# Performance work log

Hardware: AMD Instinct MI355X
Metric: run time of the kernel (lower is better)

Reference implementation:

```python
import jax, jax.numpy as jnp
import numpy as np

N = 10000   # nodes
E = 80000   # edges
B = 2       # batch
T = 12      # time steps
F_IN = 64
F_OUT = 64


def setup_inputs() -> dict:
    key = jax.random.key(0)
    ks = jax.random.split(key, 8)
    x = jax.random.normal(ks[0], (B, N, T, F_IN), dtype=jnp.float32)
    src = jax.random.randint(ks[1], (E,), 0, N)
    dst = jax.random.randint(ks[2], (E,), 0, N)
    s = 1.0 / np.sqrt(F_IN)
    W_pool = jax.random.uniform(ks[3], (F_IN, F_IN), jnp.float32, -s, s)
    b_pool = jax.random.uniform(ks[4], (F_IN,), jnp.float32, -s, s)
    W_neigh = jax.random.uniform(ks[5], (F_OUT, F_IN), jnp.float32, -s, s)
    W_self = jax.random.uniform(ks[6], (F_OUT, F_IN), jnp.float32, -s, s)
    bias = jnp.zeros((F_OUT,), jnp.float32)
    return dict(x=x, src=src, dst=dst, W_pool=W_pool, b_pool=b_pool,
                W_neigh=W_neigh, W_self=W_self, bias=bias)


def reference(x, src, dst, W_pool, b_pool, W_neigh, W_self, bias):
    # x: (B, N, T, F) -> (N, B, T, F); node dim first as SAGEConv expects
    h = jnp.transpose(x, (1, 0, 2, 3))
    # pool aggregator: per-node MLP + relu (done on nodes, then gathered per edge
    # -- identical math to gather-then-MLP since the MLP is per-node/elementwise)
    msg = jax.nn.relu(jnp.einsum('nbtf,gf->nbtg', h, W_pool) + b_pool)  # (N,B,T,F)
    m = msg[src]                                                        # (E,B,T,F) gather
    neigh = jax.ops.segment_max(m, dst, num_segments=N)                 # max-pool per dst node
    # zero-in-degree nodes get -inf from segment_max -> replace with 0 (DGL behavior)
    neigh = jnp.where(jnp.isfinite(neigh), neigh, jnp.zeros((), neigh.dtype))
    rst = (jnp.einsum('nbtf,of->nbto', h, W_self)
           + jnp.einsum('nbtf,of->nbto', neigh, W_neigh)
           + bias)                                                      # (N,B,T,F_OUT)
    return jnp.transpose(rst, (1, 0, 2, 3))                              # (B,N,T,F_OUT)
```

## Files before the change

### kernel.cpp

```cpp
#include <hip/hip_runtime.h>

#define NN 10000
#define NE 80000
#define NB 2
#define NT 12
#define NF 64
#define ROWS (NB*NN*NT)

typedef __attribute__((ext_vector_type(8))) short bf16x8;
typedef __attribute__((ext_vector_type(4))) float f32x4;

__device__ __forceinline__ unsigned short f2b(float f) {
    unsigned int u = __builtin_bit_cast(unsigned int, f);
    u += 0x7fffu + ((u >> 16) & 1u);
    return (unsigned short)(u >> 16);
}
__device__ __forceinline__ float b2f_lo(unsigned int u){ return __builtin_bit_cast(float, u << 16); }
__device__ __forceinline__ float b2f_hi(unsigned int u){ return __builtin_bit_cast(float, u & 0xffff0000u); }

__global__ __launch_bounds__(256) void k_prep(const float* __restrict__ Wp,
        const float* __restrict__ Wn, const float* __restrict__ Ws,
        unsigned short* __restrict__ Wp_b, unsigned short* __restrict__ Wcat) {
    int t = threadIdx.x;
    for (int i = t; i < 4096; i += 256) {
        Wp_b[i] = f2b(Wp[i]);
        int o = i >> 6, g = i & 63;
        Wcat[o*128 + g] = f2b(Ws[i]);
        Wcat[o*128 + 64 + ((g & 15)*4 + (g >> 4))] = f2b(Wn[i]);
    }
}

__global__ __launch_bounds__(256) void k_msg(const float* __restrict__ x,
        const unsigned short* __restrict__ Wp_b, const float* __restrict__ bp,
        unsigned short* __restrict__ msg, unsigned short* __restrict__ xb) {
    __shared__ __align__(16) unsigned short A[128*72];
    __shared__ __align__(16) unsigned short W[64*72];
    int tid = threadIdx.x;
    {
        int row = tid >> 2, c = (tid & 3) * 16;
        bf16x8 w0 = *(const bf16x8*)(Wp_b + row*64 + c);
        bf16x8 w1 = *(const bf16x8*)(Wp_b + row*64 + c + 8);
        *(bf16x8*)(W + row*72 + c)     = w0;
        *(bf16x8*)(W + row*72 + c + 8) = w1;
    }
    int m0 = blockIdx.x * 128;
    #pragma unroll
    for (int k = 0; k < 8; ++k) {
        int c = tid + 256*k;
        int row = c >> 4, f0 = (c & 15) * 4;
        float4 v = *(const float4*)(x + (size_t)(m0 + row)*64 + f0);
        uint2 p;
        p.x = f2b(v.x) | ((unsigned int)f2b(v.y) << 16);
        p.y = f2b(v.z) | ((unsigned int)f2b(v.w) << 16);
        *(uint2*)(A + row*72 + f0) = p;
        *(uint2*)(xb + (size_t)(m0 + row)*64 + f0) = p;
    }
    __syncthreads();

    int lane = tid & 63, w = tid >> 6;
    int cl = lane & 15, gq = lane >> 4;
    f32x4 acc[2][4] = {};
    #pragma unroll
    for (int kk = 0; kk < 2; ++kk) {
        int ko = kk*32 + gq*8;
        bf16x8 a0 = *(const bf16x8*)(A + (w*32 + cl)*72 + ko);
        bf16x8 a1 = *(const bf16x8*)(A + (w*32 + 16 + cl)*72 + ko);
        #pragma unroll
        for (int nf = 0; nf < 4; ++nf) {
            bf16x8 b = *(const bf16x8*)(W + (nf*16 + cl)*72 + ko);
            acc[0][nf] = __builtin_amdgcn_mfma_f32_16x16x32_bf16(a0, b, acc[0][nf], 0,0,0);
            acc[1][nf] = __builtin_amdgcn_mfma_f32_16x16x32_bf16(a1, b, acc[1][nf], 0,0,0);
        }
    }
    float bpv[4];
    #pragma unroll
    for (int nf = 0; nf < 4; ++nf) bpv[nf] = bp[nf*16 + cl];
    #pragma unroll
    for (int m = 0; m < 2; ++m)
    #pragma unroll
    for (int r = 0; r < 4; ++r) {
        int row = m0 + w*32 + m*16 + gq*4 + r;
        int b  = row / (NN*NT);
        int rem = row - b*(NN*NT);
        int node = rem / NT, t = rem - node*NT;
        float v0 = fmaxf(acc[m][0][r] + bpv[0], 0.f);
        float v1 = fmaxf(acc[m][1][r] + bpv[1], 0.f);
        float v2 = fmaxf(acc[m][2][r] + bpv[2], 0.f);
        float v3 = fmaxf(acc[m][3][r] + bpv[3], 0.f);
        uint2 p;
        p.x = f2b(v0) | ((unsigned int)f2b(v1) << 16);
        p.y = f2b(v2) | ((unsigned int)f2b(v3) << 16);
        *(uint2*)(msg + ((size_t)(node*24 + b*12 + t)*64) + cl*4) = p;
    }
}

__global__ void k_count(const int* __restrict__ dst, int* __restrict__ cnt) {
    int e = blockIdx.x * blockDim.x + threadIdx.x;
    if (e < NE) atomicAdd(&cnt[dst[e]], 1);
}

__global__ __launch_bounds__(1024) void k_scan(const int* __restrict__ cnt,
        int* __restrict__ rowptr, int* __restrict__ wofs) {
    __shared__ int s[1024];
    int tid = threadIdx.x;
    const int C = 10;
    int base = tid * C;
    int loc[C];
    int sum = 0;
    for (int i = 0; i < C; ++i) {
        int idx = base + i;
        int v = (idx < NN) ? cnt[idx] : 0;
        loc[i] = sum;
        sum += v;
    }
    s[tid] = sum;
    __syncthreads();
    for (int off = 1; off < 1024; off <<= 1) {
        int v = (tid >= off) ? s[tid - off] : 0;
        __syncthreads();
        s[tid] += v;
        __syncthreads();
    }
    int prev = (tid == 0) ? 0 : s[tid - 1];
    for (int i = 0; i < C; ++i) {
        int idx = base + i;
        if (idx < NN) {
            int v = prev + loc[i];
            rowptr[idx] = v;
            wofs[idx]   = v;
        }
    }
    if (tid == 1023) rowptr[NN] = s[1023];
}

__global__ void k_scatter(const int* __restrict__ src, const int* __restrict__ dst,
        int* __restrict__ wofs, int* __restrict__ csr) {
    int e = blockIdx.x * blockDim.x + threadIdx.x;
    if (e < NE) {
        int pos = atomicAdd(&wofs[dst[e]], 1);
        csr[pos] = src[e];
    }
}

__global__ __launch_bounds__(256, 8) void k_out(const unsigned short* __restrict__ xb,
        const unsigned short* __restrict__ msg, const unsigned short* __restrict__ Wcat,
        const float* __restrict__ bias,
        const int* __restrict__ rowptr, const int* __restrict__ csr,
        float* __restrict__ out) {
    __shared__ __align__(16) unsigned short A[32*136];
    int tid = threadIdx.x;
    int n = blockIdx.x;

    {
        int c = tid, row = c >> 4, f0 = (c & 15) * 4;
        int b = row / 12, tt = row - b*12;
        *(uint2*)(A + row*136 + f0) =
            *(const uint2*)(xb + ((size_t)(b*NN + n)*12 + tt)*64 + f0);
        if (tid < 128) {
            int c2 = tid + 256, row2 = c2 >> 4, f02 = (c2 & 15)*4;
            int b2 = row2 / 12, tt2 = row2 - b2*12;
            *(uint2*)(A + row2*136 + f02) =
                *(const uint2*)(xb + ((size_t)(b2*NN + n)*12 + tt2)*64 + f02);
        } else {
            unsigned int* z = (unsigned int*)(A + 24*136);
            int i = tid - 128;
            #pragma unroll
            for (int k = 0; k < 5; ++k) { int j = i + 128*k; if (j < 544) z[j] = 0u; }
        }
    }
    const unsigned int* msg_dw = (const unsigned int*)msg;
    int rp0 = rowptr[n], rp1 = rowptr[n + 1];
    int i0 = tid, i1 = tid + 256, i2 = tid + 512;
    float mlo[3] = {0.f,0.f,0.f}, mhi[3] = {0.f,0.f,0.f};
    int e = rp0;
    for (; e + 4 <= rp1; e += 4) {
        int s0 = csr[e]*768, s1 = csr[e+1]*768, s2 = csr[e+2]*768, s3 = csr[e+3]*768;
        unsigned int u00 = msg_dw[s0+i0], u01 = msg_dw[s0+i1], u02 = msg_dw[s0+i2];
        unsigned int u10 = msg_dw[s1+i0], u11 = msg_dw[s1+i1], u12 = msg_dw[s1+i2];
        unsigned int u20 = msg_dw[s2+i0], u21 = msg_dw[s2+i1], u22 = msg_dw[s2+i2];
        unsigned int u30 = msg_dw[s3+i0], u31 = msg_dw[s3+i1], u32 = msg_dw[s3+i2];
        mlo[0] = fmaxf(fmaxf(fmaxf(mlo[0], b2f_lo(u00)), fmaxf(b2f_lo(u10), b2f_lo(u20))), b2f_lo(u30));
        mhi[0] = fmaxf(fmaxf(fmaxf(mhi[0], b2f_hi(u00)), fmaxf(b2f_hi(u10), b2f_hi(u20))), b2f_hi(u30));
        mlo[1] = fmaxf(fmaxf(fmaxf(mlo[1], b2f_lo(u01)), fmaxf(b2f_lo(u11), b2f_lo(u21))), b2f_lo(u31));
        mhi[1] = fmaxf(fmaxf(fmaxf(mhi[1], b2f_hi(u01)), fmaxf(b2f_hi(u11), b2f_hi(u21))), b2f_hi(u31));
        mlo[2] = fmaxf(fmaxf(fmaxf(mlo[2], b2f_lo(u02)), fmaxf(b2f_lo(u12), b2f_lo(u22))), b2f_lo(u32));
        mhi[2] = fmaxf(fmaxf(fmaxf(mhi[2], b2f_hi(u02)), fmaxf(b2f_hi(u12), b2f_hi(u22))), b2f_hi(u32));
    }
    for (; e < rp1; ++e) {
        int s0 = csr[e]*768;
        unsigned int u0 = msg_dw[s0+i0], u1 = msg_dw[s0+i1], u2 = msg_dw[s0+i2];
        mlo[0] = fmaxf(mlo[0], b2f_lo(u0));  mhi[0] = fmaxf(mhi[0], b2f_hi(u0));
        mlo[1] = fmaxf(mlo[1], b2f_lo(u1));  mhi[1] = fmaxf(mhi[1], b2f_hi(u1));
        mlo[2] = fmaxf(mlo[2], b2f_lo(u2));  mhi[2] = fmaxf(mhi[2], b2f_hi(u2));
    }
    {
        unsigned int lo0 = __builtin_bit_cast(unsigned int, mlo[0]) >> 16;
        unsigned int hi0 = __builtin_bit_cast(unsigned int, mhi[0]) & 0xffff0000u;
        *(unsigned int*)(A + (i0>>5)*136 + 64 + (i0&31)*2) = hi0 | lo0;
        unsigned int lo1 = __builtin_bit_cast(unsigned int, mlo[1]) >> 16;
        unsigned int hi1 = __builtin_bit_cast(unsigned int, mhi[1]) & 0xffff0000u;
        *(unsigned int*)(A + (i1>>5)*136 + 64 + (i1&31)*2) = hi1 | lo1;
        unsigned int lo2 = __builtin_bit_cast(unsigned int, mlo[2]) >> 16;
        unsigned int hi2 = __builtin_bit_cast(unsigned int, mhi[2]) & 0xffff0000u;
        *(unsigned int*)(A + (i2>>5)*136 + 64 + (i2&31)*2) = hi2 | lo2;
    }
    __syncthreads();

    int lane = tid & 63, w = tid >> 6;
    int cl = lane & 15, gq = lane >> 4;
    f32x4 acc0 = {}, acc1 = {};
    #pragma unroll
    for (int kk = 0; kk < 4; ++kk) {
        int ko = kk*32 + gq*8;
        bf16x8 b  = *(const bf16x8*)(Wcat + (w*16 + cl)*128 + ko);
        bf16x8 a0 = *(const bf16x8*)(A + cl*136 + ko);
        bf16x8 a1 = *(const bf16x8*)(A + (16 + cl)*136 + ko);
        acc0 = __builtin_amdgcn_mfma_f32_16x16x32_bf16(a0, b, acc0, 0,0,0);
        acc1 = __builtin_amdgcn_mfma_f32_16x16x32_bf16(a1, b, acc1, 0,0,0);
    }
    float bv = bias[w*16 + cl];
    #pragma unroll
    for (int r = 0; r < 4; ++r) {
        int row = gq*4 + r;
        int b0 = row / 12, tt = row - b0*12;
        out[((size_t)(b0*NN + n)*12 + tt)*64 + w*16 + cl] = acc0[r] + bv;
    }
    if (gq < 2) {
        #pragma unroll
        for (int r = 0; r < 4; ++r) {
            int row = 16 + gq*4 + r;
            int b0 = row / 12, tt = row - b0*12;
            out[((size_t)(b0*NN + n)*12 + tt)*64 + w*16 + cl] = acc1[r] + bv;
        }
    }
}

extern "C" void kernel_launch(void* const* d_in, const int* in_sizes, int n_in,
                              void* d_out, int out_size, void* d_ws, size_t ws_size,
                              hipStream_t stream) {
    const float* x    = (const float*)d_in[0];
    const int*   src  = (const int*)  d_in[1];
    const int*   dst  = (const int*)  d_in[2];
    const float* Wp   = (const float*)d_in[3];
    const float* bp   = (const float*)d_in[4];
    const float* Wn   = (const float*)d_in[5];
    const float* Wsf  = (const float*)d_in[6];
    const float* bias = (const float*)d_in[7];
    float* out = (float*)d_out;

    char* ws = (char*)d_ws;
    int*            cnt    = (int*)           (ws);
    int*            rowptr = (int*)           (ws + 40064);
    int*            wofs   = (int*)           (ws + 80128);
    int*            csr    = (int*)           (ws + 120192);
    unsigned short* Wp_b   = (unsigned short*)(ws + 440320);
    unsigned short* Wcat   = (unsigned short*)(ws + 448512);
    unsigned short* msg    = (unsigned short*)(ws + 464896);
    unsigned short* xb     = (unsigned short*)(ws + 31184896);

    hipMemsetAsync(cnt, 0, NN * sizeof(int), stream);
    k_prep   <<<1, 256, 0, stream>>>(Wp, Wn, Wsf, Wp_b, Wcat);
    k_msg    <<<ROWS/128, 256, 0, stream>>>(x, Wp_b, bp, msg, xb);
    k_count  <<<(NE + 255) / 256, 256, 0, stream>>>(dst, cnt);
    k_scan   <<<1, 1024, 0, stream>>>(cnt, rowptr, wofs);
    k_scatter<<<(NE + 255) / 256, 256, 0, stream>>>(src, dst, wofs, csr);
    k_out    <<<NN, 256, 0, stream>>>(xb, msg, Wcat, bias, rowptr, csr, out);
}
```

Measured before the change: 107.4 us.

## Process one node per wavefront in output kernel with packed bf16 integer max

```diff
diff --git a/kernel.cpp b/kernel.cpp
--- a/kernel.cpp
+++ b/kernel.cpp
@@ -8,6 +8,7 @@
 #define ROWS (NB*NN*NT)
 
 typedef __attribute__((ext_vector_type(8))) short bf16x8;
+typedef __attribute__((ext_vector_type(8))) unsigned short u16x8;
 typedef __attribute__((ext_vector_type(4))) float f32x4;
 
 __device__ __forceinline__ unsigned short f2b(float f) {
@@ -15,8 +16,6 @@
     u += 0x7fffu + ((u >> 16) & 1u);
     return (unsigned short)(u >> 16);
 }
-__device__ __forceinline__ float b2f_lo(unsigned int u){ return __builtin_bit_cast(float, u << 16); }
-__device__ __forceinline__ float b2f_hi(unsigned int u){ return __builtin_bit_cast(float, u & 0xffff0000u); }
 
 __global__ __launch_bounds__(256) void k_prep(const float* __restrict__ Wp,
         const float* __restrict__ Wn, const float* __restrict__ Ws,
@@ -48,12 +47,16 @@
     for (int k = 0; k < 8; ++k) {
         int c = tid + 256*k;
         int row = c >> 4, f0 = (c & 15) * 4;
-        float4 v = *(const float4*)(x + (size_t)(m0 + row)*64 + f0);
+        int grow = m0 + row;
+        float4 v = *(const float4*)(x + (size_t)grow*64 + f0);
         uint2 p;
         p.x = f2b(v.x) | ((unsigned int)f2b(v.y) << 16);
         p.y = f2b(v.z) | ((unsigned int)f2b(v.w) << 16);
         *(uint2*)(A + row*72 + f0) = p;
-        *(uint2*)(xb + (size_t)(m0 + row)*64 + f0) = p;
+        int b = grow / (NN*NT);
+        int rem = grow - b*(NN*NT);
+        int node = rem / NT, t = rem - node*NT;
+        *(uint2*)(xb + ((size_t)node*24 + b*12 + t)*64 + f0) = p;
     }
     __syncthreads();
 
@@ -83,10 +86,10 @@
         int b  = row / (NN*NT);
         int rem = row - b*(NN*NT);
         int node = rem / NT, t = rem - node*NT;
-        float v0 = fmaxf(acc[m][0][r] + bpv[0], 0.f);
-        float v1 = fmaxf(acc[m][1][r] + bpv[1], 0.f);
-        float v2 = fmaxf(acc[m][2][r] + bpv[2], 0.f);
-        float v3 = fmaxf(acc[m][3][r] + bpv[3], 0.f);
+        float v0 = fmaxf(acc[m][0][r] + bpv[0], 0.f) + 0.0f;
+        float v1 = fmaxf(acc[m][1][r] + bpv[1], 0.f) + 0.0f;
+        float v2 = fmaxf(acc[m][2][r] + bpv[2], 0.f) + 0.0f;
+        float v3 = fmaxf(acc[m][3][r] + bpv[3], 0.f) + 0.0f;
         uint2 p;
         p.x = f2b(v0) | ((unsigned int)f2b(v1) << 16);
         p.y = f2b(v2) | ((unsigned int)f2b(v3) << 16);
@@ -142,95 +145,93 @@
     }
 }
 
-__global__ __launch_bounds__(256, 8) void k_out(const unsigned short* __restrict__ xb,
+__global__ __launch_bounds__(256, 4) void k_out(const unsigned short* __restrict__ xb,
         const unsigned short* __restrict__ msg, const unsigned short* __restrict__ Wcat,
         const float* __restrict__ bias,
         const int* __restrict__ rowptr, const int* __restrict__ csr,
         float* __restrict__ out) {
-    __shared__ __align__(16) unsigned short A[32*136];
+    __shared__ __align__(16) unsigned short NL[4*24*72 + 8*72];
     int tid = threadIdx.x;
-    int n = blockIdx.x;
-
-    {
-        int c = tid, row = c >> 4, f0 = (c & 15) * 4;
-        int b = row / 12, tt = row - b*12;
-        *(uint2*)(A + row*136 + f0) =
-            *(const uint2*)(xb + ((size_t)(b*NN + n)*12 + tt)*64 + f0);
-        if (tid < 128) {
-            int c2 = tid + 256, row2 = c2 >> 4, f02 = (c2 & 15)*4;
-            int b2 = row2 / 12, tt2 = row2 - b2*12;
-            *(uint2*)(A + row2*136 + f02) =
-                *(const uint2*)(xb + ((size_t)(b2*NN + n)*12 + tt2)*64 + f02);
-        } else {
-            unsigned int* z = (unsigned int*)(A + 24*136);
-            int i = tid - 128;
-            #pragma unroll
-            for (int k = 0; k < 5; ++k) { int j = i + 128*k; if (j < 544) z[j] = 0u; }
-        }
-    }
-    const unsigned int* msg_dw = (const unsigned int*)msg;
+    int w = tid >> 6, lane = tid & 63;
+    int n = blockIdx.x * 4 + w;
+    unsigned short* tile = NL + w * (24*72);
+    int cl = lane & 15, gq = lane >> 4;
+
+    const unsigned short* xrow = xb + (size_t)n * 1536;
+    bf16x8 a_self[2][2];
+    #pragma unroll
+    for (int kk = 0; kk < 2; ++kk) {
+        int ko = kk*32 + gq*8;
+        a_self[0][kk] = *(const bf16x8*)(xrow + cl*64 + ko);
+        a_self[1][kk] = *(const bf16x8*)(xrow + (16 + cl)*64 + ko);
+    }
+
+    const u16x8* __restrict__ m8 = (const u16x8*)msg;
     int rp0 = rowptr[n], rp1 = rowptr[n + 1];
-    int i0 = tid, i1 = tid + 256, i2 = tid + 512;
-    float mlo[3] = {0.f,0.f,0.f}, mhi[3] = {0.f,0.f,0.f};
+    u16x8 mx0 = {}, mx1 = {}, mx2 = {};
     int e = rp0;
     for (; e + 4 <= rp1; e += 4) {
-        int s0 = csr[e]*768, s1 = csr[e+1]*768, s2 = csr[e+2]*768, s3 = csr[e+3]*768;
-        unsigned int u00 = msg_dw[s0+i0], u01 = msg_dw[s0+i1], u02 = msg_dw[s0+i2];
-        unsigned int u10 = msg_dw[s1+i0], u11 = msg_dw[s1+i1], u12 = msg_dw[s1+i2];
-        unsigned int u20 = msg_dw[s2+i0], u21 = msg_dw[s2+i1], u22 = msg_dw[s2+i2];
-        unsigned int u30 = msg_dw[s3+i0], u31 = msg_dw[s3+i1], u32 = msg_dw[s3+i2];
-        mlo[0] = fmaxf(fmaxf(fmaxf(mlo[0], b2f_lo(u00)), fmaxf(b2f_lo(u10), b2f_lo(u20))), b2f_lo(u30));
-        mhi[0] = fmaxf(fmaxf(fmaxf(mhi[0], b2f_hi(u00)), fmaxf(b2f_hi(u10), b2f_hi(u20))), b2f_hi(u30));
-        mlo[1] = fmaxf(fmaxf(fmaxf(mlo[1], b2f_lo(u01)), fmaxf(b2f_lo(u11), b2f_lo(u21))), b2f_lo(u31));
-        mhi[1] = fmaxf(fmaxf(fmaxf(mhi[1], b2f_hi(u01)), fmaxf(b2f_hi(u11), b2f_hi(u21))), b2f_hi(u31));
-        mlo[2] = fmaxf(fmaxf(fmaxf(mlo[2], b2f_lo(u02)), fmaxf(b2f_lo(u12), b2f_lo(u22))), b2f_lo(u32));
-        mhi[2] = fmaxf(fmaxf(fmaxf(mhi[2], b2f_hi(u02)), fmaxf(b2f_hi(u12), b2f_hi(u22))), b2f_hi(u32));
+        int s0 = csr[e]*192, s1 = csr[e+1]*192, s2 = csr[e+2]*192, s3 = csr[e+3]*192;
+        u16x8 v00 = m8[s0+lane], v01 = m8[s0+64+lane], v02 = m8[s0+128+lane];
+        u16x8 v10 = m8[s1+lane], v11 = m8[s1+64+lane], v12 = m8[s1+128+lane];
+        u16x8 v20 = m8[s2+lane], v21 = m8[s2+64+lane], v22 = m8[s2+128+lane];
+        u16x8 v30 = m8[s3+lane], v31 = m8[s3+64+lane], v32 = m8[s3+128+lane];
+        mx0 = __builtin_elementwise_max(__builtin_elementwise_max(mx0, v00),
+              __builtin_elementwise_max(__builtin_elementwise_max(v10, v20), v30));
+        mx1 = __builtin_elementwise_max(__builtin_elementwise_max(mx1, v01),
+              __builtin_elementwise_max(__builtin_elementwise_max(v11, v21), v31));
+        mx2 = __builtin_elementwise_max(__builtin_elementwise_max(mx2, v02),
+              __builtin_elementwise_max(__builtin_elementwise_max(v12, v22), v32));
     }
     for (; e < rp1; ++e) {
-        int s0 = csr[e]*768;
-        unsigned int u0 = msg_dw[s0+i0], u1 = msg_dw[s0+i1], u2 = msg_dw[s0+i2];
-        mlo[0] = fmaxf(mlo[0], b2f_lo(u0));  mhi[0] = fmaxf(mhi[0], b2f_hi(u0));
-        mlo[1] = fmaxf(mlo[1], b2f_lo(u1));  mhi[1] = fmaxf(mhi[1], b2f_hi(u1));
-        mlo[2] = fmaxf(mlo[2], b2f_lo(u2));  mhi[2] = fmaxf(mhi[2], b2f_hi(u2));
-    }
-    {
-        unsigned int lo0 = __builtin_bit_cast(unsigned int, mlo[0]) >> 16;
-        unsigned int hi0 = __builtin_bit_cast(unsigned int, mhi[0]) & 0xffff0000u;
-        *(unsigned int*)(A + (i0>>5)*136 + 64 + (i0&31)*2) = hi0 | lo0;
-        unsigned int lo1 = __builtin_bit_cast(unsigned int, mlo[1]) >> 16;
-        unsigned int hi1 = __builtin_bit_cast(unsigned int, mhi[1]) & 0xffff0000u;
-        *(unsigned int*)(A + (i1>>5)*136 + 64 + (i1&31)*2) = hi1 | lo1;
-        unsigned int lo2 = __builtin_bit_cast(unsigned int, mlo[2]) >> 16;
-        unsigned int hi2 = __builtin_bit_cast(unsigned int, mhi[2]) & 0xffff0000u;
-        *(unsigned int*)(A + (i2>>5)*136 + 64 + (i2&31)*2) = hi2 | lo2;
-    }
-    __syncthreads();
-
-    int lane = tid & 63, w = tid >> 6;
-    int cl = lane & 15, gq = lane >> 4;
-    f32x4 acc0 = {}, acc1 = {};
+        int s0 = csr[e]*192;
+        mx0 = __builtin_elementwise_max(mx0, m8[s0+lane]);
+        mx1 = __builtin_elementwise_max(mx1, m8[s0+64+lane]);
+        mx2 = __builtin_elementwise_max(mx2, m8[s0+128+lane]);
+    }
+    *(u16x8*)(tile + (0  + (lane>>3))*72 + (lane&7)*8) = mx0;
+    *(u16x8*)(tile + (8  + (lane>>3))*72 + (lane&7)*8) = mx1;
+    *(u16x8*)(tile + (16 + (lane>>3))*72 + (lane&7)*8) = mx2;
+
+    f32x4 acc0[4] = {}, acc1[4] = {};
     #pragma unroll
     for (int kk = 0; kk < 4; ++kk) {
-        int ko = kk*32 + gq*8;
-        bf16x8 b  = *(const bf16x8*)(Wcat + (w*16 + cl)*128 + ko);
-        bf16x8 a0 = *(const bf16x8*)(A + cl*136 + ko);
-        bf16x8 a1 = *(const bf16x8*)(A + (16 + cl)*136 + ko);
-        acc0 = __builtin_amdgcn_mfma_f32_16x16x32_bf16(a0, b, acc0, 0,0,0);
-        acc1 = __builtin_amdgcn_mfma_f32_16x16x32_bf16(a1, b, acc1, 0,0,0);
-    }
-    float bv = bias[w*16 + cl];
-    #pragma unroll
-    for (int r = 0; r < 4; ++r) {
-        int row = gq*4 + r;
-        int b0 = row / 12, tt = row - b0*12;
-        out[((size_t)(b0*NN + n)*12 + tt)*64 + w*16 + cl] = acc0[r] + bv;
+        bf16x8 a0, a1;
+        if (kk < 2) { a0 = a_self[0][kk]; a1 = a_self[1][kk]; }
+        else {
+            int ko = (kk - 2)*32 + gq*8;
+            a0 = *(const bf16x8*)(tile + cl*72 + ko);
+            a1 = *(const bf16x8*)(tile + (16 + cl)*72 + ko);
+        }
+        #pragma unroll
+        for (int cg = 0; cg < 4; ++cg) {
+            bf16x8 b = *(const bf16x8*)(Wcat + (cg*16 + cl)*128 + kk*32 + gq*8);
+            acc0[cg] = __builtin_amdgcn_mfma_f32_16x16x32_bf16(a0, b, acc0[cg], 0,0,0);
+            acc1[cg] = __builtin_amdgcn_mfma_f32_16x16x32_bf16(a1, b, acc1[cg], 0,0,0);
+        }
+    }
+    #pragma unroll
+    for (int cg = 0; cg < 4; ++cg) {
+        float bv = bias[cg*16 + cl];
+        #pragma unroll
+        for (int r = 0; r < 4; ++r) {
+            int row = gq*4 + r;
+            int b0 = row / 12, tt = row - b0*12;
+            __builtin_nontemporal_store(acc0[cg][r] + bv,
+                out + ((size_t)(b0*NN + n)*12 + tt)*64 + cg*16 + cl);
+        }
     }
     if (gq < 2) {
         #pragma unroll
-        for (int r = 0; r < 4; ++r) {
-            int row = 16 + gq*4 + r;
-            int b0 = row / 12, tt = row - b0*12;
-            out[((size_t)(b0*NN + n)*12 + tt)*64 + w*16 + cl] = acc1[r] + bv;
+        for (int cg = 0; cg < 4; ++cg) {
+            float bv = bias[cg*16 + cl];
+            #pragma unroll
+            for (int r = 0; r < 4; ++r) {
+                int row = 16 + gq*4 + r;
+                int b0 = row / 12, tt = row - b0*12;
+                __builtin_nontemporal_store(acc1[cg][r] + bv,
+                    out + ((size_t)(b0*NN + n)*12 + tt)*64 + cg*16 + cl);
+            }
         }
     }
 }
@@ -255,8 +256,8 @@
     int*            csr    = (int*)           (ws + 120192);
     unsigned short* Wp_b   = (unsigned short*)(ws + 440320);
     unsigned short* Wcat   = (unsigned short*)(ws + 448512);
-    unsigned short* msg    = (unsigned short*)(ws + 464896);
-    unsigned short* xb     = (unsigned short*)(ws + 31184896);
+    unsigned short* xb     = (unsigned short*)(ws + 464896);
+    unsigned short* msg    = (unsigned short*)(ws + 31184896);
 
     hipMemsetAsync(cnt, 0, NN * sizeof(int), stream);
     k_prep   <<<1, 256, 0, stream>>>(Wp, Wn, Wsf, Wp_b, Wcat);
@@ -264,5 +265,5 @@
     k_count  <<<(NE + 255) / 256, 256, 0, stream>>>(dst, cnt);
     k_scan   <<<1, 1024, 0, stream>>>(cnt, rowptr, wofs);
     k_scatter<<<(NE + 255) / 256, 256, 0, stream>>>(src, dst, wofs, csr);
-    k_out    <<<NN, 256, 0, stream>>>(xb, msg, Wcat, bias, rowptr, csr, out);
-}
+    k_out    <<<NN/4, 256, 0, stream>>>(xb, msg, Wcat, bias, rowptr, csr, out);
+}
```

Result: no change. 109.5 us (+1.9%).
